# Performance work log

Measured on AMD Instinct MI355X. Metric: run time of the kernel, lower is better.

The kernel has to match this reference:

```python
import jax, jax.numpy as jnp
import numpy as np

B, S, I, H, O, L = 32, 512, 1024, 1024, 1024, 2


def setup_inputs() -> dict:
    key = jax.random.key(0)
    ks = jax.random.split(key, 14)
    s = 0.02  # weight init scale
    inp = {
        "x": jax.random.normal(ks[0], (B, S, I), dtype=jnp.float32),
        "h0": jnp.zeros((B, L, H), dtype=jnp.float32),
        # z gate: Linear(in,h,bias=True) for x, Linear(h,h,bias=False) for h
        "Wzx": jax.random.normal(ks[1], (L, H, I), dtype=jnp.float32) * s,
        "bz": jnp.zeros((L, H), dtype=jnp.float32),
        "Wzh": jax.random.normal(ks[2], (L, H, H), dtype=jnp.float32) * s,
        # r gate
        "Wrx": jax.random.normal(ks[3], (L, H, I), dtype=jnp.float32) * s,
        "br": jnp.zeros((L, H), dtype=jnp.float32),
        "Wrh": jax.random.normal(ks[4], (L, H, H), dtype=jnp.float32) * s,
        # g candidate
        "Wgx": jax.random.normal(ks[5], (L, H, I), dtype=jnp.float32) * s,
        "bg": jnp.zeros((L, H), dtype=jnp.float32),
        "Wgh": jax.random.normal(ks[6], (L, H, H), dtype=jnp.float32) * s,
        # output projection Linear(h, out, bias=True)
        "Wo": jax.random.normal(ks[7], (O, H), dtype=jnp.float32) * s,
        "bo": jnp.zeros((O,), dtype=jnp.float32),
    }
    return inp


def reference(x, h0, Wzx, bz, Wzh, Wrx, br, Wrh, Wgx, bg, Wgh, Wo, bo):
    n_layers = Wzx.shape[0]

    def step(h, x_t):
        # h: [L, B, H] layer hidden states; x_t: [B, I] input at timestep t
        new_h = []
        inp = x_t
        for k in range(n_layers):
            hk = h[k]
            z = jax.nn.sigmoid(inp @ Wzx[k].T + bz[k] + hk @ Wzh[k].T)
            r = jax.nn.sigmoid(inp @ Wrx[k].T + br[k] + hk @ Wrh[k].T)
            g = jnp.tanh(inp @ Wgx[k].T + bg[k] + (r * hk) @ Wgh[k].T)
            hk = (1.0 - z) * hk + z * g
            new_h.append(hk)
            inp = hk  # dropout=0 -> identity
        y_t = inp @ Wo.T + bo  # [B, O]
        return jnp.stack(new_h), y_t

    h_init = jnp.transpose(h0, (1, 0, 2))  # [L, B, H]
    xs = jnp.swapaxes(x, 0, 1)             # [S, B, I]
    h_final, ys = jax.lax.scan(step, h_init, xs)
    layer_output = jnp.swapaxes(ys, 0, 1)          # [B, S, O]
    hidden_state = jnp.transpose(h_final, (1, 0, 2))  # [B, L, H]
    return layer_output, hidden_state
```

## Files before the change

kernel.cpp:

```cpp
#include <hip/hip_runtime.h>
#include <hip/hip_bf16.h>
#include <cstdio>
#include <cstdint>


typedef float f32x4 __attribute__((ext_vector_type(4)));
typedef __bf16 bf16x8 __attribute__((ext_vector_type(8)));
typedef unsigned short u16;

#define AS1 __attribute__((address_space(1)))
#define AS3 __attribute__((address_space(3)))

__device__ inline u16 f2b(float f) {
  __hip_bfloat16 h = __float2bfloat16(f);
  return *reinterpret_cast<u16*>(&h);
}
__device__ inline float b2f(u16 u) {
  __hip_bfloat16 h;
  *reinterpret_cast<u16*>(&h) = u;
  return __bfloat162float(h);
}
__device__ inline bf16x8 ld8(const u16* p) {
  return *reinterpret_cast<const bf16x8*>(p);
}
__device__ inline f32x4 mfma16(bf16x8 a, bf16x8 b, f32x4 c) {
  return __builtin_amdgcn_mfma_f32_16x16x32_bf16(a, b, c, 0, 0, 0);
}

__device__ inline void gload_lds16(const void* g, void* l) {
  __builtin_amdgcn_global_load_lds((const AS1 void*)g, (AS3 void*)l, 16, 0, 0);
}
__device__ inline void gload_lds16c(const void* g, void* l) {
  __builtin_amdgcn_global_load_lds((const AS1 void*)g, (AS3 void*)l, 16, 0, 0x10);
}

__device__ inline void st16(u16* p, u16 v) {
  __hip_atomic_store(p, v, __ATOMIC_RELAXED, __HIP_MEMORY_SCOPE_AGENT);
}

__device__ inline void poll64(unsigned* f, unsigned target, int lane) {
  unsigned* p = f + lane;
  while (true) {
    unsigned v = __hip_atomic_load(p, __ATOMIC_RELAXED, __HIP_MEMORY_SCOPE_AGENT);
    if (__all((int)(v >= target))) break;
    __builtin_amdgcn_s_sleep(1);
  }
}

__device__ inline void poll64x2(unsigned* fa, unsigned ta, unsigned* fb,
                                unsigned tb, int lane) {
  unsigned* pa = fa + lane;
  unsigned* pb = fb + lane;
  while (true) {
    unsigned va = __hip_atomic_load(pa, __ATOMIC_RELAXED, __HIP_MEMORY_SCOPE_AGENT);
    unsigned vb = __hip_atomic_load(pb, __ATOMIC_RELAXED, __HIP_MEMORY_SCOPE_AGENT);
    if (__all((int)(va >= ta) & (int)(vb >= tb))) break;
    __builtin_amdgcn_s_sleep(1);
  }
}


__global__ void castk(const float* __restrict__ src, u16* __restrict__ dst, int n) {
  int i = blockIdx.x * 256 + threadIdx.x;
  if (i < n) dst[i] = f2b(src[i]);
}

__global__ void init_h(const float* __restrict__ h0, float* __restrict__ h32_0,
                       float* __restrict__ h32_1, u16* __restrict__ hring_s3,
                       u16* __restrict__ hbf_1) {
  int i = blockIdx.x * 256 + threadIdx.x;
  if (i < 32 * 1024) {
    int b = i >> 10, j = i & 1023;
    float v0 = h0[(b * 2 + 0) * 1024 + j];
    float v1 = h0[(b * 2 + 1) * 1024 + j];
    h32_0[i] = v0; hring_s3[i] = f2b(v0);
    h32_1[i] = v1; hbf_1[i] = f2b(v1);
  }
}

__global__ void final_h(const float* __restrict__ h32_0, const float* __restrict__ h32_1,
                        float* __restrict__ out) {
  int i = blockIdx.x * 256 + threadIdx.x;
  if (i < 32 * 1024) {
    int b = i >> 10, j = i & 1023;
    out[(b * 2 + 0) * 1024 + j] = h32_0[i];
    out[(b * 2 + 1) * 1024 + j] = h32_1[i];
  }
}


template <int MODE>
__global__ __launch_bounds__(256, 2) void gemm_nt(const u16* __restrict__ A,
                                                  const u16* __restrict__ B,
                                                  const float* __restrict__ bias,
                                                  void* __restrict__ Cout,
                                                  int M, int N, int K) {
  __shared__ __align__(16) u16 As[128 * 32];
  __shared__ __align__(16) u16 Bs[128 * 32];
  const int tid = threadIdx.x;
  const int lane = tid & 63;
  const int wave = tid >> 6;
  const int tilesN = N >> 7;
  const int bm = blockIdx.x / tilesN, bn = blockIdx.x % tilesN;
  const int wr = (wave >> 1) << 6, wc = (wave & 1) << 6;
  const int la = lane & 15, kg = lane >> 4;
  f32x4 acc[4][4] = {};
  const int srow = tid >> 2, skoff = (tid & 3) << 3;
  const u16* Ap = A + (size_t)(bm * 128 + srow) * K + skoff;
  const u16* Bp = B + (size_t)(bn * 128 + srow) * K + skoff;
  for (int k0 = 0; k0 < K; k0 += 32) {
    gload_lds16(Ap + k0,            As + tid * 8);
    gload_lds16(Ap + (size_t)64 * K + k0, As + 2048 + tid * 8);
    gload_lds16(Bp + k0,            Bs + tid * 8);
    gload_lds16(Bp + (size_t)64 * K + k0, Bs + 2048 + tid * 8);
    __syncthreads();
    bf16x8 af[4], bfr[4];
#pragma unroll
    for (int i = 0; i < 4; ++i) af[i] = ld8(As + (wr + i * 16 + la) * 32 + kg * 8);
#pragma unroll
    for (int j = 0; j < 4; ++j) bfr[j] = ld8(Bs + (wc + j * 16 + la) * 32 + kg * 8);
#pragma unroll
    for (int i = 0; i < 4; ++i)
#pragma unroll
      for (int j = 0; j < 4; ++j)
        acc[i][j] = mfma16(af[i], bfr[j], acc[i][j]);
    __syncthreads();
  }
  const int rbase = bm * 128 + wr + kg * 4;
  const int cbase = bn * 128 + wc + la;
#pragma unroll
  for (int i = 0; i < 4; ++i) {
#pragma unroll
    for (int j = 0; j < 4; ++j) {
      int col = cbase + j * 16;
      float bv = bias[col];
#pragma unroll
      for (int e = 0; e < 4; ++e) {
        int row = rbase + i * 16 + e;
        float v = acc[i][j][e] + bv;
        if (MODE == 0) {
          ((float*)Cout)[(size_t)row * N + col] = v;
        } else {
          int tt = row & 511, bb = row >> 9;
          ((u16*)Cout)[((size_t)(tt * 32 + bb)) * N + col] = f2b(v);
        }
      }
    }
  }
}


__global__ __launch_bounds__(128, 1) void gru_pipe2(
    const u16* __restrict__ Wz0, const u16* __restrict__ Wr0, const u16* __restrict__ Wg0,
    const u16* __restrict__ Wz1, const u16* __restrict__ Wr1, const u16* __restrict__ Wg1,
    const u16* __restrict__ Wzx1, const u16* __restrict__ Wrx1, const u16* __restrict__ Wgx1,
    const float* __restrict__ bz1, const float* __restrict__ br1, const float* __restrict__ bg1,
    const u16* __restrict__ Az, const u16* __restrict__ Ar, const u16* __restrict__ Ag,
    u16* __restrict__ hring, u16* __restrict__ hist1,
    float* __restrict__ h32_0, float* __restrict__ h32_1,
    u16* __restrict__ hbf1,
    u16* __restrict__ rhbf0, u16* __restrict__ rhbf1,
    unsigned* __restrict__ flags, int S) {
  __shared__ __align__(16) u16 LDSh[16 * 1024];
  __shared__ __align__(16) u16 LDSx[16 * 1024];
  __shared__ __align__(16) u16 WXZ[32 * 1024];
  __shared__ float zloc[256];
  __shared__ float h32loc[256];
  __shared__ float part[256];
  const int tid = threadIdx.x, wave = tid >> 6, lane = tid & 63;
  const int la = lane & 15, kg = lane >> 4;
  const int sw = la & 7;
  const int layer = blockIdx.x >> 7;
  const int rt = (blockIdx.x >> 6) & 1, colT = blockIdx.x & 63;
  const int col = colT * 16 + la;
  unsigned* myfl1 = flags + (layer * 2 + rt) * 128;
  unsigned* myfl2 = myfl1 + 64;
  unsigned* l1fl1 = flags + (2 + rt) * 128;
  unsigned* l0fl2 = flags + rt * 128 + 64;

  float* h32g = layer ? h32_1 : h32_0;
  u16* rhbf = layer ? rhbf1 : rhbf0;

  for (int i = tid; i < 256; i += 128)
    h32loc[i] = h32g[(rt * 16 + (i >> 4)) * 1024 + colT * 16 + (i & 15)];

  const u16* w1p = (wave ? (layer ? Wr1 : Wr0) : (layer ? Wz1 : Wz0)) +
                   (size_t)col * 1024 + kg * 8;
  const u16* wgp = (layer ? Wg1 : Wg0) + (size_t)col * 1024 + wave * 512 + kg * 8;
  bf16x8 wzr[32], wg[16];
#pragma unroll
  for (int ks = 0; ks < 32; ++ks) wzr[ks] = ld8(w1p + ks * 32);
#pragma unroll
  for (int ks = 0; ks < 16; ++ks) wg[ks] = ld8(wgp + ks * 32);

  bf16x8 wgx[16];
  float b1v = 0.f, bgv = 0.f;
  if (layer) {
    const u16* wxp = (wave ? Wrx1 : Wzx1) + (size_t)col * 1024 + kg * 8;
#pragma unroll
    for (int ks = 0; ks < 32; ++ks) {
      bf16x8 w = ld8(wxp + ks * 32);
      *reinterpret_cast<bf16x8*>(&WXZ[((wave * 32 + ks) * 64 + lane) * 8]) = w;
    }
    const u16* wgxp = Wgx1 + (size_t)col * 1024 + wave * 512 + kg * 8;
#pragma unroll
    for (int ks = 0; ks < 16; ++ks) wgx[ks] = ld8(wgxp + ks * 32);
    b1v = wave ? br1[col] : bz1[col];
    bgv = bg1[col];
  }
  __syncthreads();

  const u16* wxl = WXZ + (wave * 32 * 64 + lane) * 8;
  const u16* A1 = wave ? Ar : Az;
  const u16* rsrc = rhbf + rt * 16384;
  const int rowb = rt * 16 + kg * 4;

  for (int t = 0; t < S; ++t) {
    u16 a1raw[4] = {0, 0, 0, 0};
    u16 agraw[4] = {0, 0, 0, 0};
    if (!layer) {
      const u16* A1t = A1 + (size_t)t * 32768;
#pragma unroll
      for (int e = 0; e < 4; ++e) a1raw[e] = A1t[(rowb + e) * 1024 + col];
      if (wave == 0) {
        const u16* Agt = Ag + (size_t)t * 32768;
#pragma unroll
        for (int e = 0; e < 4; ++e) agraw[e] = Agt[(rowb + e) * 1024 + col];
      }
      unsigned tb = t >= 4 ? (unsigned)(t - 3) : 0u;
      poll64x2(myfl2, (unsigned)t, l1fl1, tb, lane);
    } else {
      poll64x2(myfl2, (unsigned)t, l0fl2, (unsigned)(t + 1), lane);
      const u16* xs = hring + (t & 3) * 32768 + rt * 16384;
#pragma unroll
      for (int i = 0; i < 16; ++i) {
        int u = i * 2 + wave, r = u >> 1, c = u & 1;
        gload_lds16c(xs + r * 1024 + c * 512 + (lane ^ (r & 7)) * 8,
                     LDSx + r * 1024 + c * 512 + lane * 8);
      }
    }
    const u16* hs = layer ? (hbf1 + rt * 16384)
                          : (hring + ((t + 3) & 3) * 32768 + rt * 16384);
#pragma unroll
    for (int i = 0; i < 16; ++i) {
      int u = i * 2 + wave, r = u >> 1, c = u & 1;
      gload_lds16c(hs + r * 1024 + c * 512 + (lane ^ (r & 7)) * 8,
                   LDSh + r * 1024 + c * 512 + lane * 8);
    }
    __syncthreads();
    f32x4 p0 = {0.f, 0.f, 0.f, 0.f}, p1 = {0.f, 0.f, 0.f, 0.f};
#pragma unroll
    for (int ks = 0; ks < 32; ks += 2) {
      p0 = mfma16(ld8(LDSh + la * 1024 + (((ks * 4 + kg) ^ sw) << 3)), wzr[ks], p0);
      p1 = mfma16(ld8(LDSh + la * 1024 + ((((ks + 1) * 4 + kg) ^ sw) << 3)), wzr[ks + 1], p1);
    }
    if (layer) {
#pragma unroll
      for (int ks = 0; ks < 32; ks += 2) {
        p0 = mfma16(ld8(LDSx + la * 1024 + (((ks * 4 + kg) ^ sw) << 3)),
                    ld8(wxl + ks * 512), p0);
        p1 = mfma16(ld8(LDSx + la * 1024 + ((((ks + 1) * 4 + kg) ^ sw) << 3)),
                    ld8(wxl + (ks + 1) * 512), p1);
      }
    }
    if (wave == 0) {
#pragma unroll
      for (int e = 0; e < 4; ++e) {
        float pre = p0[e] + p1[e] + (layer ? b1v : b2f(a1raw[e]));
        zloc[(kg * 4 + e) * 16 + la] = 1.f / (1.f + __expf(-pre));
      }
    } else {
#pragma unroll
      for (int e = 0; e < 4; ++e) {
        float pre = p0[e] + p1[e] + (layer ? b1v : b2f(a1raw[e]));
        float rv = 1.f / (1.f + __expf(-pre));
        st16(&rhbf[(rowb + e) * 1024 + col], f2b(rv * h32loc[(kg * 4 + e) * 16 + la]));
      }
      __builtin_amdgcn_s_waitcnt(0);
      if (lane == 0)
        __hip_atomic_store(&myfl1[colT], (unsigned)(t + 1), __ATOMIC_RELAXED,
                           __HIP_MEMORY_SCOPE_AGENT);
    }
    __syncthreads();
    poll64(myfl1, (unsigned)(t + 1), lane);
#pragma unroll
    for (int i = 0; i < 16; ++i) {
      int u = i * 2 + wave, r = u >> 1, c = u & 1;
      gload_lds16c(rsrc + r * 1024 + c * 512 + (lane ^ (r & 7)) * 8,
                   LDSh + r * 1024 + c * 512 + lane * 8);
    }
    __syncthreads();
    f32x4 q0 = {0.f, 0.f, 0.f, 0.f}, q1 = {0.f, 0.f, 0.f, 0.f};
#pragma unroll
    for (int ks = 0; ks < 16; ks += 2) {
      q0 = mfma16(ld8(LDSh + la * 1024 + (((wave * 64 + ks * 4 + kg) ^ sw) << 3)), wg[ks], q0);
      q1 = mfma16(ld8(LDSh + la * 1024 + (((wave * 64 + (ks + 1) * 4 + kg) ^ sw) << 3)), wg[ks + 1], q1);
    }
    if (layer) {
#pragma unroll
      for (int ks = 0; ks < 16; ks += 2) {
        q0 = mfma16(ld8(LDSx + la * 1024 + (((wave * 64 + ks * 4 + kg) ^ sw) << 3)), wgx[ks], q0);
        q1 = mfma16(ld8(LDSx + la * 1024 + (((wave * 64 + (ks + 1) * 4 + kg) ^ sw) << 3)), wgx[ks + 1], q1);
      }
    }
    if (wave == 1) {
#pragma unroll
      for (int e = 0; e < 4; ++e) part[lane * 4 + e] = q0[e] + q1[e];
    }
    __syncthreads();
    if (wave == 0) {
      float hnv[4];
      u16 hbv[4];
      u16* hdst = layer ? hbf1 : (hring + (t & 3) * 32768);
#pragma unroll
      for (int e = 0; e < 4; ++e) {
        int li = (kg * 4 + e) * 16 + la;
        float gs = q0[e] + q1[e] + part[lane * 4 + e] + (layer ? bgv : b2f(agraw[e]));
        float ex = __expf(2.f * gs);
        float g = 1.f - 2.f / (ex + 1.f);
        float z = zloc[li];
        float hn = (1.f - z) * h32loc[li] + z * g;
        h32loc[li] = hn;
        hnv[e] = hn;
        hbv[e] = f2b(hn);
        st16(&hdst[(rowb + e) * 1024 + col], hbv[e]);
      }
      __builtin_amdgcn_s_waitcnt(0);
      if (lane == 0)
        __hip_atomic_store(&myfl2[colT], (unsigned)(t + 1), __ATOMIC_RELAXED,
                           __HIP_MEMORY_SCOPE_AGENT);
#pragma unroll
      for (int e = 0; e < 4; ++e) {
        if (layer) hist1[((size_t)(rowb + e) * S + t) * 1024 + col] = hbv[e];
        if (t == S - 1) h32g[(rowb + e) * 1024 + col] = hnv[e];
      }
    }
    __syncthreads();
  }
}


extern "C" void kernel_launch(void* const* d_in, const int* in_sizes, int n_in,
                              void* d_out, int out_size, void* d_ws, size_t ws_size,
                              hipStream_t stream) {
  (void)in_sizes; (void)n_in; (void)out_size;
  const float* x   = (const float*)d_in[0];
  const float* h0  = (const float*)d_in[1];
  const float* Wzx = (const float*)d_in[2];
  const float* bz  = (const float*)d_in[3];
  const float* Wzh = (const float*)d_in[4];
  const float* Wrx = (const float*)d_in[5];
  const float* br  = (const float*)d_in[6];
  const float* Wrh = (const float*)d_in[7];
  const float* Wgx = (const float*)d_in[8];
  const float* bg  = (const float*)d_in[9];
  const float* Wgh = (const float*)d_in[10];
  const float* Wo  = (const float*)d_in[11];
  const float* bo  = (const float*)d_in[12];
  float* out = (float*)d_out;
  char* ws = (char*)d_ws;

  const size_t MB = 1024 * 1024;
  size_t o = 4096;
  u16* wWzx = (u16*)(ws + o); o += 4 * MB;
  u16* wWzh = (u16*)(ws + o); o += 4 * MB;
  u16* wWrx = (u16*)(ws + o); o += 4 * MB;
  u16* wWrh = (u16*)(ws + o); o += 4 * MB;
  u16* wWgx = (u16*)(ws + o); o += 4 * MB;
  u16* wWgh = (u16*)(ws + o); o += 4 * MB;
  u16* wWo  = (u16*)(ws + o); o += 2 * MB;
  u16* Az    = (u16*)(ws + o); o += 32 * MB;
  u16* Ar    = (u16*)(ws + o); o += 32 * MB;
  u16* Ag    = (u16*)(ws + o); o += 32 * MB;
  u16* hring = (u16*)(ws + o); o += 256 * 1024;
  u16* xbf   = (u16*)(ws + o); o += 32 * MB;
  float* h32_0 = (float*)(ws + o); o += 131072;
  float* h32_1 = (float*)(ws + o); o += 131072;
  u16* hbf_1 = (u16*)(ws + o); o += 65536;
  u16* rhbf0 = (u16*)(ws + o); o += 65536;
  u16* rhbf1 = (u16*)(ws + o); o += 65536;

  if (ws_size < o) {
    fprintf(stderr, "[gru] INSUFFICIENT WORKSPACE ws=%zu need=%zu\n", ws_size, o);
    return;
  }
  unsigned* flags = (unsigned*)ws;
  hipMemsetAsync(ws, 0, 4096, stream);

  castk<<<dim3(8192), dim3(256), 0, stream>>>(Wzx, wWzx, 2097152);
  castk<<<dim3(8192), dim3(256), 0, stream>>>(Wzh, wWzh, 2097152);
  castk<<<dim3(8192), dim3(256), 0, stream>>>(Wrx, wWrx, 2097152);
  castk<<<dim3(8192), dim3(256), 0, stream>>>(Wrh, wWrh, 2097152);
  castk<<<dim3(8192), dim3(256), 0, stream>>>(Wgx, wWgx, 2097152);
  castk<<<dim3(8192), dim3(256), 0, stream>>>(Wgh, wWgh, 2097152);
  castk<<<dim3(4096), dim3(256), 0, stream>>>(Wo, wWo, 1048576);
  castk<<<dim3(65536), dim3(256), 0, stream>>>(x, xbf, 16777216);
  init_h<<<dim3(128), dim3(256), 0, stream>>>(h0, h32_0, h32_1,
                                              hring + 3 * 32768, hbf_1);

  gemm_nt<2><<<dim3(1024), dim3(256), 0, stream>>>(xbf, wWzx, bz, Az, 16384, 1024, 1024);
  gemm_nt<2><<<dim3(1024), dim3(256), 0, stream>>>(xbf, wWrx, br, Ar, 16384, 1024, 1024);
  gemm_nt<2><<<dim3(1024), dim3(256), 0, stream>>>(xbf, wWgx, bg, Ag, 16384, 1024, 1024);

  gru_pipe2<<<dim3(256), dim3(128), 0, stream>>>(
      wWzh, wWrh, wWgh,
      wWzh + 1048576, wWrh + 1048576, wWgh + 1048576,
      wWzx + 1048576, wWrx + 1048576, wWgx + 1048576,
      bz + 1024, br + 1024, bg + 1024,
      Az, Ar, Ag, hring, xbf,
      h32_0, h32_1, hbf_1, rhbf0, rhbf1,
      flags, 512);

  gemm_nt<0><<<dim3(1024), dim3(256), 0, stream>>>(xbf, wWo, bo, out, 16384, 1024, 1024);

  final_h<<<dim3(128), dim3(256), 0, stream>>>(h32_0, h32_1, out + 16777216);
}
```

Measured before the change: 6.541 ms.

## Split GRU recurrent step across four waves with LDS partial-sum reduction

Doubles the persistent GRU block from two to four waves. Layer-1 input weights now sit in registers of the extra waves instead of being streamed from shared memory, and layer 0 splits the K dimension across waves. Partial sums are combined through a shared `part` array, which needs an extra barrier after the z/r phase, while two other barriers are dropped. The aim is to shorten the serial per-timestep latency by spreading the MFMA work and removing LDS weight reads, at the cost of more cross-wave reductions and synchronisation.

```diff
diff --git a/kernel.cpp b/kernel.cpp
--- a/kernel.cpp
+++ b/kernel.cpp
@@ -150,7 +150,7 @@
 }
 
 
-__global__ __launch_bounds__(128, 1) void gru_pipe2(
+__global__ __launch_bounds__(256, 1) void gru_pipe3(
     const u16* __restrict__ Wz0, const u16* __restrict__ Wr0, const u16* __restrict__ Wg0,
     const u16* __restrict__ Wz1, const u16* __restrict__ Wr1, const u16* __restrict__ Wg1,
     const u16* __restrict__ Wzx1, const u16* __restrict__ Wrx1, const u16* __restrict__ Wgx1,
@@ -163,10 +163,9 @@
     unsigned* __restrict__ flags, int S) {
   __shared__ __align__(16) u16 LDSh[16 * 1024];
   __shared__ __align__(16) u16 LDSx[16 * 1024];
-  __shared__ __align__(16) u16 WXZ[32 * 1024];
+  __shared__ float part[4][256];
   __shared__ float zloc[256];
   __shared__ float h32loc[256];
-  __shared__ float part[256];
   const int tid = threadIdx.x, wave = tid >> 6, lane = tid & 63;
   const int la = lane & 15, kg = lane >> 4;
   const int sw = la & 7;
@@ -181,37 +180,43 @@
   float* h32g = layer ? h32_1 : h32_0;
   u16* rhbf = layer ? rhbf1 : rhbf0;
 
-  for (int i = tid; i < 256; i += 128)
-    h32loc[i] = h32g[(rt * 16 + (i >> 4)) * 1024 + colT * 16 + (i & 15)];
-
-  const u16* w1p = (wave ? (layer ? Wr1 : Wr0) : (layer ? Wz1 : Wz0)) +
-                   (size_t)col * 1024 + kg * 8;
-  const u16* wgp = (layer ? Wg1 : Wg0) + (size_t)col * 1024 + wave * 512 + kg * 8;
-  bf16x8 wzr[32], wg[16];
-#pragma unroll
-  for (int ks = 0; ks < 32; ++ks) wzr[ks] = ld8(w1p + ks * 32);
-#pragma unroll
-  for (int ks = 0; ks < 16; ++ks) wg[ks] = ld8(wgp + ks * 32);
-
-  bf16x8 wgx[16];
+  h32loc[tid] = h32g[(rt * 16 + (tid >> 4)) * 1024 + colT * 16 + (tid & 15)];
+
+  bf16x8 wzr[32];
+  if (layer) {
+    const u16* wsrc;
+    if (wave == 0) wsrc = Wz1;
+    else if (wave == 1) wsrc = Wr1;
+    else if (wave == 2) wsrc = Wzx1;
+    else wsrc = Wrx1;
+    const u16* wp = wsrc + (size_t)col * 1024 + kg * 8;
+#pragma unroll
+    for (int ks = 0; ks < 32; ++ks) wzr[ks] = ld8(wp + ks * 32);
+  } else {
+    const u16* wsrc = (wave & 1) ? Wr0 : Wz0;
+    const u16* wp = wsrc + (size_t)col * 1024 + kg * 8 + (size_t)(wave >> 1) * 512;
+#pragma unroll
+    for (int ks = 0; ks < 16; ++ks) wzr[ks] = ld8(wp + ks * 32);
+  }
+  bf16x8 wg[16];
+  if (layer) {
+    const u16* wsrc = (wave < 2) ? Wg1 : Wgx1;
+    const u16* wp = wsrc + (size_t)col * 1024 + kg * 8 + (size_t)(wave & 1) * 512;
+#pragma unroll
+    for (int ks = 0; ks < 16; ++ks) wg[ks] = ld8(wp + ks * 32);
+  } else {
+    const u16* wp = Wg0 + (size_t)col * 1024 + kg * 8 + (size_t)wave * 256;
+#pragma unroll
+    for (int ks = 0; ks < 8; ++ks) wg[ks] = ld8(wp + ks * 32);
+  }
   float b1v = 0.f, bgv = 0.f;
   if (layer) {
-    const u16* wxp = (wave ? Wrx1 : Wzx1) + (size_t)col * 1024 + kg * 8;
-#pragma unroll
-    for (int ks = 0; ks < 32; ++ks) {
-      bf16x8 w = ld8(wxp + ks * 32);
-      *reinterpret_cast<bf16x8*>(&WXZ[((wave * 32 + ks) * 64 + lane) * 8]) = w;
-    }
-    const u16* wgxp = Wgx1 + (size_t)col * 1024 + wave * 512 + kg * 8;
-#pragma unroll
-    for (int ks = 0; ks < 16; ++ks) wgx[ks] = ld8(wgxp + ks * 32);
-    b1v = wave ? br1[col] : bz1[col];
-    bgv = bg1[col];
+    if (wave == 0) { b1v = bz1[col]; bgv = bg1[col]; }
+    else if (wave == 1) b1v = br1[col];
   }
   __syncthreads();
 
-  const u16* wxl = WXZ + (wave * 32 * 64 + lane) * 8;
-  const u16* A1 = wave ? Ar : Az;
+  const u16* A1 = (wave == 1) ? Ar : Az;
   const u16* rsrc = rhbf + rt * 16384;
   const int rowb = rt * 16 + kg * 4;
 
@@ -219,9 +224,11 @@
     u16 a1raw[4] = {0, 0, 0, 0};
     u16 agraw[4] = {0, 0, 0, 0};
     if (!layer) {
-      const u16* A1t = A1 + (size_t)t * 32768;
-#pragma unroll
-      for (int e = 0; e < 4; ++e) a1raw[e] = A1t[(rowb + e) * 1024 + col];
+      if (wave < 2) {
+        const u16* A1t = A1 + (size_t)t * 32768;
+#pragma unroll
+        for (int e = 0; e < 4; ++e) a1raw[e] = A1t[(rowb + e) * 1024 + col];
+      }
       if (wave == 0) {
         const u16* Agt = Ag + (size_t)t * 32768;
 #pragma unroll
@@ -233,8 +240,8 @@
       poll64x2(myfl2, (unsigned)t, l0fl2, (unsigned)(t + 1), lane);
       const u16* xs = hring + (t & 3) * 32768 + rt * 16384;
 #pragma unroll
-      for (int i = 0; i < 16; ++i) {
-        int u = i * 2 + wave, r = u >> 1, c = u & 1;
+      for (int i = 0; i < 8; ++i) {
+        int u = i * 4 + wave, r = u >> 1, c = u & 1;
         gload_lds16c(xs + r * 1024 + c * 512 + (lane ^ (r & 7)) * 8,
                      LDSx + r * 1024 + c * 512 + lane * 8);
       }
@@ -242,37 +249,45 @@
     const u16* hs = layer ? (hbf1 + rt * 16384)
                           : (hring + ((t + 3) & 3) * 32768 + rt * 16384);
 #pragma unroll
-    for (int i = 0; i < 16; ++i) {
-      int u = i * 2 + wave, r = u >> 1, c = u & 1;
+    for (int i = 0; i < 8; ++i) {
+      int u = i * 4 + wave, r = u >> 1, c = u & 1;
       gload_lds16c(hs + r * 1024 + c * 512 + (lane ^ (r & 7)) * 8,
                    LDSh + r * 1024 + c * 512 + lane * 8);
     }
     __syncthreads();
     f32x4 p0 = {0.f, 0.f, 0.f, 0.f}, p1 = {0.f, 0.f, 0.f, 0.f};
-#pragma unroll
-    for (int ks = 0; ks < 32; ks += 2) {
-      p0 = mfma16(ld8(LDSh + la * 1024 + (((ks * 4 + kg) ^ sw) << 3)), wzr[ks], p0);
-      p1 = mfma16(ld8(LDSh + la * 1024 + ((((ks + 1) * 4 + kg) ^ sw) << 3)), wzr[ks + 1], p1);
-    }
     if (layer) {
+      const u16* aB = (wave >= 2) ? LDSx : LDSh;
 #pragma unroll
       for (int ks = 0; ks < 32; ks += 2) {
-        p0 = mfma16(ld8(LDSx + la * 1024 + (((ks * 4 + kg) ^ sw) << 3)),
-                    ld8(wxl + ks * 512), p0);
-        p1 = mfma16(ld8(LDSx + la * 1024 + ((((ks + 1) * 4 + kg) ^ sw) << 3)),
-                    ld8(wxl + (ks + 1) * 512), p1);
-      }
-    }
+        p0 = mfma16(ld8(aB + la * 1024 + (((ks * 4 + kg) ^ sw) << 3)), wzr[ks], p0);
+        p1 = mfma16(ld8(aB + la * 1024 + ((((ks + 1) * 4 + kg) ^ sw) << 3)), wzr[ks + 1], p1);
+      }
+    } else {
+      const int ko = (wave >> 1) * 16;
+#pragma unroll
+      for (int ks = 0; ks < 16; ks += 2) {
+        p0 = mfma16(ld8(LDSh + la * 1024 + ((((ko + ks) * 4 + kg) ^ sw) << 3)), wzr[ks], p0);
+        p1 = mfma16(ld8(LDSh + la * 1024 + ((((ko + ks + 1) * 4 + kg) ^ sw) << 3)), wzr[ks + 1], p1);
+      }
+    }
+    if (wave >= 2) {
+#pragma unroll
+      for (int e = 0; e < 4; ++e) part[wave][lane * 4 + e] = p0[e] + p1[e];
+    }
+    __syncthreads();
     if (wave == 0) {
 #pragma unroll
       for (int e = 0; e < 4; ++e) {
-        float pre = p0[e] + p1[e] + (layer ? b1v : b2f(a1raw[e]));
+        float pre = p0[e] + p1[e] + part[2][lane * 4 + e] +
+                    (layer ? b1v : b2f(a1raw[e]));
         zloc[(kg * 4 + e) * 16 + la] = 1.f / (1.f + __expf(-pre));
       }
-    } else {
+    } else if (wave == 1) {
 #pragma unroll
       for (int e = 0; e < 4; ++e) {
-        float pre = p0[e] + p1[e] + (layer ? b1v : b2f(a1raw[e]));
+        float pre = p0[e] + p1[e] + part[3][lane * 4 + e] +
+                    (layer ? b1v : b2f(a1raw[e]));
         float rv = 1.f / (1.f + __expf(-pre));
         st16(&rhbf[(rowb + e) * 1024 + col], f2b(rv * h32loc[(kg * 4 + e) * 16 + la]));
       }
@@ -281,31 +296,34 @@
         __hip_atomic_store(&myfl1[colT], (unsigned)(t + 1), __ATOMIC_RELAXED,
                            __HIP_MEMORY_SCOPE_AGENT);
     }
-    __syncthreads();
     poll64(myfl1, (unsigned)(t + 1), lane);
 #pragma unroll
-    for (int i = 0; i < 16; ++i) {
-      int u = i * 2 + wave, r = u >> 1, c = u & 1;
+    for (int i = 0; i < 8; ++i) {
+      int u = i * 4 + wave, r = u >> 1, c = u & 1;
       gload_lds16c(rsrc + r * 1024 + c * 512 + (lane ^ (r & 7)) * 8,
                    LDSh + r * 1024 + c * 512 + lane * 8);
     }
     __syncthreads();
     f32x4 q0 = {0.f, 0.f, 0.f, 0.f}, q1 = {0.f, 0.f, 0.f, 0.f};
-#pragma unroll
-    for (int ks = 0; ks < 16; ks += 2) {
-      q0 = mfma16(ld8(LDSh + la * 1024 + (((wave * 64 + ks * 4 + kg) ^ sw) << 3)), wg[ks], q0);
-      q1 = mfma16(ld8(LDSh + la * 1024 + (((wave * 64 + (ks + 1) * 4 + kg) ^ sw) << 3)), wg[ks + 1], q1);
-    }
     if (layer) {
+      const u16* aB = (wave >= 2) ? LDSx : LDSh;
+      const int ko = (wave & 1) * 16;
 #pragma unroll
       for (int ks = 0; ks < 16; ks += 2) {
-        q0 = mfma16(ld8(LDSx + la * 1024 + (((wave * 64 + ks * 4 + kg) ^ sw) << 3)), wgx[ks], q0);
-        q1 = mfma16(ld8(LDSx + la * 1024 + (((wave * 64 + (ks + 1) * 4 + kg) ^ sw) << 3)), wgx[ks + 1], q1);
-      }
-    }
-    if (wave == 1) {
-#pragma unroll
-      for (int e = 0; e < 4; ++e) part[lane * 4 + e] = q0[e] + q1[e];
+        q0 = mfma16(ld8(aB + la * 1024 + ((((ko + ks) * 4 + kg) ^ sw) << 3)), wg[ks], q0);
+        q1 = mfma16(ld8(aB + la * 1024 + ((((ko + ks + 1) * 4 + kg) ^ sw) << 3)), wg[ks + 1], q1);
+      }
+    } else {
+      const int ko = wave * 8;
+#pragma unroll
+      for (int ks = 0; ks < 8; ks += 2) {
+        q0 = mfma16(ld8(LDSh + la * 1024 + ((((ko + ks) * 4 + kg) ^ sw) << 3)), wg[ks], q0);
+        q1 = mfma16(ld8(LDSh + la * 1024 + ((((ko + ks + 1) * 4 + kg) ^ sw) << 3)), wg[ks + 1], q1);
+      }
+    }
+    if (wave != 0) {
+#pragma unroll
+      for (int e = 0; e < 4; ++e) part[wave][lane * 4 + e] = q0[e] + q1[e];
     }
     __syncthreads();
     if (wave == 0) {
@@ -315,7 +333,9 @@
 #pragma unroll
       for (int e = 0; e < 4; ++e) {
         int li = (kg * 4 + e) * 16 + la;
-        float gs = q0[e] + q1[e] + part[lane * 4 + e] + (layer ? bgv : b2f(agraw[e]));
+        int pi = lane * 4 + e;
+        float gs = q0[e] + q1[e] + part[1][pi] + part[2][pi] + part[3][pi] +
+                   (layer ? bgv : b2f(agraw[e]));
         float ex = __expf(2.f * gs);
         float g = 1.f - 2.f / (ex + 1.f);
         float z = zloc[li];
@@ -335,7 +355,6 @@
         if (t == S - 1) h32g[(rowb + e) * 1024 + col] = hnv[e];
       }
     }
-    __syncthreads();
   }
 }
 
@@ -402,7 +421,7 @@
   gemm_nt<2><<<dim3(1024), dim3(256), 0, stream>>>(xbf, wWrx, br, Ar, 16384, 1024, 1024);
   gemm_nt<2><<<dim3(1024), dim3(256), 0, stream>>>(xbf, wWgx, bg, Ag, 16384, 1024, 1024);
 
-  gru_pipe2<<<dim3(256), dim3(128), 0, stream>>>(
+  gru_pipe3<<<dim3(256), dim3(256), 0, stream>>>(
       wWzh, wWrh, wWgh,
       wWzh + 1048576, wWrh + 1048576, wWgh + 1048576,
       wWzx + 1048576, wWrx + 1048576, wWgx + 1048576,
```

Result: no change. 6.569 ms (+0.4%).
